# Optimization experiments

Hardware: AMD Instinct MI355X
Metric: run time of the kernel (lower is better)

Reference implementation:

```python
import jax, jax.numpy as jnp
import numpy as np

RANK = 3
NUM_STEPS = 3
NUM_ENT = 40000
NUM_EMB = 24
NUM_OPS = 12
DIM = 128
HID = 128
BATCH = 128
NNZ = 300000


def _lstm_dir(x, Wih, Whh, bih, bhh, reverse=False):
    # x: (S, B, D); PyTorch gate order i, f, g, o
    B = x.shape[1]
    H = Whh.shape[1]
    def step(carry, xt):
        h, c = carry
        z = xt @ Wih.T + h @ Whh.T + bih + bhh  # (B, 4H)
        i, f, g, o = jnp.split(z, 4, axis=-1)
        c = jax.nn.sigmoid(f) * c + jax.nn.sigmoid(i) * jnp.tanh(g)
        h = jax.nn.sigmoid(o) * jnp.tanh(c)
        return (h, c), h
    init = (jnp.zeros((B, H), x.dtype), jnp.zeros((B, H), x.dtype))
    _, hs = jax.lax.scan(step, init, x, reverse=reverse)
    return hs  # (S, B, H)


def _spmm(memory, src, dst, val, num_ent):
    # memory: (B, E); edges (src -> dst): out[b, j] = sum_{e: dst[e]=j} memory[b, src[e]] * val[e]
    g = memory[:, src] * val[None, :]              # (B, nnz)
    out = jax.ops.segment_sum(g.T, dst, num_segments=num_ent)  # (E, B)
    return out.T


def setup_inputs() -> dict:
    key = jax.random.key(0)
    ks = jax.random.split(key, 16)
    inp = {
        'queries': jax.random.randint(ks[0], (BATCH,), 0, NUM_EMB),
        'heads': jax.random.randint(ks[1], (BATCH,), 0, NUM_ENT),
        'edge_src': jax.random.randint(ks[2], (NUM_OPS, NNZ), 0, NUM_ENT, dtype=jnp.int32),
        'edge_dst': jax.random.randint(ks[3], (NUM_OPS, NNZ), 0, NUM_ENT, dtype=jnp.int32),
        'edge_val': jax.random.uniform(ks[4], (NUM_OPS, NNZ), jnp.float32),
        'emb': jax.random.normal(ks[5], (NUM_EMB, DIM), jnp.float32) * 0.1,
        'Wih_f': jax.random.normal(ks[6], (RANK, 4 * HID, DIM), jnp.float32) * 0.1,
        'Whh_f': jax.random.normal(ks[7], (RANK, 4 * HID, HID), jnp.float32) * 0.1,
        'bih_f': jnp.zeros((RANK, 4 * HID), jnp.float32),
        'bhh_f': jnp.zeros((RANK, 4 * HID), jnp.float32),
        'Wih_b': jax.random.normal(ks[8], (RANK, 4 * HID, DIM), jnp.float32) * 0.1,
        'Whh_b': jax.random.normal(ks[9], (RANK, 4 * HID, HID), jnp.float32) * 0.1,
        'bih_b': jnp.zeros((RANK, 4 * HID), jnp.float32),
        'bhh_b': jnp.zeros((RANK, 4 * HID), jnp.float32),
        'W0': jax.random.normal(ks[10], (2 * HID, NUM_OPS + 1), jnp.float32) * 0.1,
        'b0': jnp.zeros((1, NUM_OPS + 1), jnp.float32),
    }
    return inp


def reference(queries, heads, edge_src, edge_dst, edge_val, emb,
              Wih_f, Whh_f, bih_f, bhh_f, Wih_b, Whh_b, bih_b, bhh_b, W0, b0):
    # query embedding replicated over time: (S, B, D)
    q = emb[queries]
    x = jnp.broadcast_to(q[None], (NUM_STEPS, q.shape[0], q.shape[1]))
    head_onehot = jax.nn.one_hot(heads, NUM_ENT, dtype=jnp.float32)  # (B, E)

    logits = jnp.zeros((q.shape[0], NUM_ENT), jnp.float32)
    for r in range(RANK):
        hf = _lstm_dir(x, Wih_f[r], Whh_f[r], bih_f[r], bhh_f[r], reverse=False)
        hb = _lstm_dir(x, Wih_b[r], Whh_b[r], bih_b[r], bhh_b[r], reverse=True)
        rnn_out = jnp.concatenate([hf, hb], axis=-1)          # (S, B, 2H)
        trans = rnn_out @ W0 + b0                             # (S, B, ops+1)
        attn = jax.nn.softmax(trans, axis=-1)
        attn = jnp.transpose(attn, (0, 2, 1))                 # (S, ops+1, B)

        memory = head_onehot                                  # (B, E)
        for t in range(NUM_STEPS):
            attn_t = attn[t]                                  # (ops+1, B)
            acc = memory * attn_t[-1][:, None]                # identity operator
            for op in range(NUM_OPS):
                prod = _spmm(memory, edge_src[op], edge_dst[op], edge_val[op], NUM_ENT)
                acc = acc + prod * attn_t[op][:, None]
            memory = acc
        norm = jnp.maximum(jnp.float32(1e-20), jnp.sum(memory, axis=1, keepdims=True))
        logits = logits + memory / norm
    return logits
```

## Files before the change

### kernel.cpp

```cpp
#include <hip/hip_runtime.h>

#define NENT 40000
#define NB 128
#define NQ 24
#define NOPS 12
#define EPO 300000
#define NTOT (NOPS * EPO)
#define NRANK 3
#define NPASS 8
#define CP 16
#define ECAP 160

typedef float v4f __attribute__((ext_vector_type(4)));

__device__ __forceinline__ v4f shfl_xor4(v4f x, int m) {
    v4f r;
    r.x = __shfl_xor(x.x, m);
    r.y = __shfl_xor(x.y, m);
    r.z = __shfl_xor(x.z, m);
    r.w = __shfl_xor(x.w, m);
    return r;
}

__device__ __forceinline__ bool bittest(const unsigned* bm, int i) {
    return (bm[i >> 5] >> (i & 31)) & 1u;
}

__global__ void headmark_kernel(const int* __restrict__ heads, unsigned* __restrict__ bmH,
                                unsigned* __restrict__ bm2) {
    int h = heads[threadIdx.x];
    atomicOr(&bmH[h >> 5], 1u << (h & 31));
    atomicOr(&bm2[h >> 5], 1u << (h & 31));
}

__global__ void mark2_kernel(const int* __restrict__ src, const int* __restrict__ dst,
                             const unsigned* __restrict__ bmH, unsigned* __restrict__ bm2) {
    int i = blockIdx.x * 256 + threadIdx.x;
    if (i < NTOT) {
        int s = src[i];
        if (bittest(bmH, s)) {
            int d = dst[i];
            atomicOr(&bm2[d >> 5], 1u << (d & 31));
        }
    }
}

__global__ void build_ell_kernel(const int* __restrict__ src, const int* __restrict__ dst,
                                 const float* __restrict__ val, const unsigned* __restrict__ bm2,
                                 int* __restrict__ fillD, int* __restrict__ fillS,
                                 int2* __restrict__ eD, int2* __restrict__ eS) {
    int i = blockIdx.x * 256 + threadIdx.x;
    if (i >= NTOT) return;
    int s = src[i], d = dst[i];
    int op = i / EPO;
    int v = __float_as_int(val[i]);
    int pd = atomicAdd(&fillD[d], 1);
    eD[(size_t)d * ECAP + pd] = make_int2(s | (op << 16), v);
    if (bittest(bm2, s)) {
        int ps = atomicAdd(&fillS[s], 1);
        eS[(size_t)s * ECAP + ps] = make_int2(d | (op << 16), v);
    }
}

__global__ void zxq_kernel(const float* __restrict__ emb,
                           const float* __restrict__ Wih_f, const float* __restrict__ bih_f,
                           const float* __restrict__ bhh_f,
                           const float* __restrict__ Wih_b, const float* __restrict__ bih_b,
                           const float* __restrict__ bhh_b,
                           float* __restrict__ zxq) {
    int combo = blockIdx.x / NQ;
    int q = blockIdx.x % NQ;
    int dir = combo / 3, r = combo % 3;
    const float* Wih = (dir ? Wih_b : Wih_f) + r * 512 * 128;
    const float* bih = (dir ? bih_b : bih_f) + r * 512;
    const float* bhh = (dir ? bhh_b : bhh_f) + r * 512;
    __shared__ float x[128];
    int u = threadIdx.x;
    x[u] = emb[q * 128 + u];
    __syncthreads();
    const float* W0p = Wih + u * 128;
    const float* W1p = Wih + (128 + u) * 128;
    const float* W2p = Wih + (256 + u) * 128;
    const float* W3p = Wih + (384 + u) * 128;
    float a0 = 0.f, a1 = 0.f, a2 = 0.f, a3 = 0.f;
    for (int d = 0; d < 128; ++d) {
        float xv = x[d];
        a0 = fmaf(xv, W0p[d], a0);
        a1 = fmaf(xv, W1p[d], a1);
        a2 = fmaf(xv, W2p[d], a2);
        a3 = fmaf(xv, W3p[d], a3);
    }
    float* o = zxq + (size_t)(combo * NQ + q) * 512;
    o[u]       = a0 + bih[u]       + bhh[u];
    o[128 + u] = a1 + bih[128 + u] + bhh[128 + u];
    o[256 + u] = a2 + bih[256 + u] + bhh[256 + u];
    o[384 + u] = a3 + bih[384 + u] + bhh[384 + u];
}

__global__ void lstmq_kernel(const float* __restrict__ Whh_f, const float* __restrict__ Whh_b,
                             const float* __restrict__ zxq, float* __restrict__ hq) {
    int combo = blockIdx.x / NQ;
    int q = blockIdx.x % NQ;
    int dir = combo / 3, r = combo % 3;
    const float* Whh = (dir ? Whh_b : Whh_f) + r * 512 * 128;
    __shared__ float h[128];
    int u = threadIdx.x;
    const float* z = zxq + (size_t)(combo * NQ + q) * 512;
    float zi0 = z[u], zf0 = z[128 + u], zg0 = z[256 + u], zo0 = z[384 + u];
    const float* Wi = Whh + u * 128;
    const float* Wf = Whh + (128 + u) * 128;
    const float* Wg = Whh + (256 + u) * 128;
    const float* Wo = Whh + (384 + u) * 128;
    float c = 0.f;
    h[u] = 0.f;
    for (int s = 0; s < 3; ++s) {
        __syncthreads();
        float a0 = 0.f, a1 = 0.f, a2 = 0.f, a3 = 0.f;
        for (int d = 0; d < 128; ++d) {
            float hv = h[d];
            a0 = fmaf(hv, Wi[d], a0);
            a1 = fmaf(hv, Wf[d], a1);
            a2 = fmaf(hv, Wg[d], a2);
            a3 = fmaf(hv, Wo[d], a3);
        }
        float ig = 1.f / (1.f + expf(-(zi0 + a0)));
        float fg = 1.f / (1.f + expf(-(zf0 + a1)));
        float gg = tanhf(zg0 + a2);
        float og = 1.f / (1.f + expf(-(zo0 + a3)));
        c = fg * c + ig * gg;
        float hn = og * tanhf(c);
        __syncthreads();
        h[u] = hn;
        hq[(size_t)((combo * 3 + s) * NQ + q) * 128 + u] = hn;
    }
}

__global__ void attnq_kernel(const float* __restrict__ hq, const float* __restrict__ W0,
                             const float* __restrict__ b0, float* __restrict__ attnq) {
    int r = blockIdx.x / 3, t = blockIdx.x % 3;
    __shared__ float W0s[256 * 13];
    for (int idx = threadIdx.x; idx < 256 * 13; idx += 32) W0s[idx] = W0[idx];
    __syncthreads();
    int q = threadIdx.x;
    if (q >= NQ) return;
    float acc[13];
    for (int k = 0; k < 13; ++k) acc[k] = b0[k];
    const float* hf = hq + (size_t)(((0 * 3 + r) * 3 + t) * NQ + q) * 128;
    const float* hb = hq + (size_t)(((1 * 3 + r) * 3 + (2 - t)) * NQ + q) * 128;
    for (int u = 0; u < 128; ++u) {
        float v = hf[u];
        for (int k = 0; k < 13; ++k) acc[k] = fmaf(v, W0s[u * 13 + k], acc[k]);
    }
    for (int u = 0; u < 128; ++u) {
        float v = hb[u];
        for (int k = 0; k < 13; ++k) acc[k] = fmaf(v, W0s[(128 + u) * 13 + k], acc[k]);
    }
    float m = acc[0];
    for (int k = 1; k < 13; ++k) m = fmaxf(m, acc[k]);
    float e[13];
    float sum = 0.f;
    for (int k = 0; k < 13; ++k) { e[k] = expf(acc[k] - m); sum += e[k]; }
    float inv = 1.f / sum;
    float* ao = attnq + (size_t)(r * 3 + t) * 13 * NQ;
    for (int k = 0; k < 13; ++k) ao[k * NQ + q] = e[k] * inv;
}

__global__ void expand_kernel(const int* __restrict__ queries, const float* __restrict__ attnq,
                              float* __restrict__ attn) {
    __shared__ int qs[128];
    if (threadIdx.x < 128) qs[threadIdx.x] = queries[threadIdx.x];
    __syncthreads();
    for (int idx = threadIdx.x; idx < 9 * 13 * 128; idx += 256) {
        int b = idx & 127, kk = idx >> 7;
        attn[idx] = attnq[kk * NQ + qs[b]];
    }
}

__global__ void fused01_kernel(const int* __restrict__ heads, const float* __restrict__ attn,
                               const int* __restrict__ fillS, const int2* __restrict__ eS,
                               float* __restrict__ mem2) {
    int r = blockIdx.y;
    int b = blockIdx.x;
    int chunk = blockIdx.z;
    __shared__ float c0s[13], c1s[13];
    if (threadIdx.x < 13) {
        c0s[threadIdx.x] = attn[(size_t)((r * 3 + 0) * 13 + threadIdx.x) * 128 + b];
        c1s[threadIdx.x] = attn[(size_t)((r * 3 + 1) * 13 + threadIdx.x) * 128 + b];
    }
    __syncthreads();
    int h = heads[b];
    int lenH = fillS[h];
    float* mem = mem2 + ((size_t)(r * NPASS + (b >> 4)) * NENT) * CP + (b & 15);
    int g = threadIdx.x >> 3, lane8 = threadIdx.x & 7;
    for (int ent = g + chunk * 32; ent < lenH + 1; ent += 64) {
        int i; float wv;
        if (ent == 0) { i = h; wv = c0s[12]; }
        else {
            int2 e = eS[(size_t)h * ECAP + ent - 1];
            i = e.x & 0xFFFF;
            wv = __int_as_float(e.y) * c0s[e.x >> 16];
        }
        if (lane8 == 0) atomicAdd(&mem[(size_t)i * CP], c1s[12] * wv);
        int lenI = fillS[i];
        const int2* ei = eS + (size_t)i * ECAP;
        for (int f = lane8; f < lenI; f += 8) {
            int2 e2 = ei[f];
            atomicAdd(&mem[(size_t)(e2.x & 0xFFFF) * CP],
                      __int_as_float(e2.y) * c1s[e2.x >> 16] * wv);
        }
    }
}

struct Stage { v4f g0, g1, g2, g3; float w0, w1, w2, w3; int o0, o1, o2, o3; };

#define ISSUE_ONE(G, W, O, LT, RT, bi) { \
    bool m = (bi) < (LT); \
    int2 e = eL[RT][m ? (bi) : 0]; \
    int ex = m ? e.x : 0; \
    W = m ? __int_as_float(e.y) : 0.f; \
    O = ex >> 16; \
    G = *(const v4f*)(inr + (size_t)(ex & 0xFFFF) * CP + cq4); }

#define ISSUE(S, bb) { int bi = (bb) + slot; \
    ISSUE_ONE(S.g0, S.w0, S.o0, l0, rw + 0, bi) \
    ISSUE_ONE(S.g1, S.w1, S.o1, l1, rw + 1, bi) \
    ISSUE_ONE(S.g2, S.w2, S.o2, l2, rw + 2, bi) \
    ISSUE_ONE(S.g3, S.w3, S.o3, l3, rw + 3, bi) }

#define CONSUME(S) { \
    { v4f cc = *(const v4f*)&cs[S.o0 * 20 + cq4]; acc0 += (S.w0 * cc) * S.g0; } \
    { v4f cc = *(const v4f*)&cs[S.o1 * 20 + cq4]; acc1 += (S.w1 * cc) * S.g1; } \
    { v4f cc = *(const v4f*)&cs[S.o2 * 20 + cq4]; acc2 += (S.w2 * cc) * S.g2; } \
    { v4f cc = *(const v4f*)&cs[S.o3 * 20 + cq4]; acc3 += (S.w3 * cc) * S.g3; } }

#define REDUCE_ROW(A, T) { \
    v4f red = A; \
    red += shfl_xor4(red, 4); \
    red += shfl_xor4(red, 8); \
    red += shfl_xor4(red, 16); \
    red += shfl_xor4(red, 32); \
    if (slot == 0) { \
        int j = jw + (T); \
        v4f mi = *(const v4f*)(inr + (size_t)j * CP + cq4); \
        v4f res = cid * mi + red; \
        *(v4f*)(outr + (size_t)j * CP + cq4) = res; \
        rsum += res; \
    } }

__global__ __launch_bounds__(256) void dense_kernel(const float* __restrict__ attn,
                                                    const int* __restrict__ fillD,
                                                    const int2* __restrict__ edgesD,
                                                    const float* __restrict__ in,
                                                    float* __restrict__ out,
                                                    float* __restrict__ normv) {
    int p = blockIdx.x;
    int r = blockIdx.z;
    __shared__ __align__(16) float cs[13 * 20];
    __shared__ float npart[4][16];
    __shared__ __align__(16) int2 eL[16][ECAP];
    int tid = threadIdx.x;
    int wave = tid >> 6, lane = tid & 63;

    {
        const char* gp = (const char*)(edgesD + (size_t)(blockIdx.y * 16) * ECAP);
        char* lp = (char*)&eL[0][0];
#pragma unroll
        for (int k = 0; k < 5; ++k) {
            int off = (wave * 5 + k) * 1024;
            __builtin_amdgcn_global_load_lds(
                (const __attribute__((address_space(1))) unsigned*)(gp + off + lane * 16),
                (__attribute__((address_space(3))) unsigned*)(lp + off),
                16, 0, 0);
        }
    }
    if (tid < 13 * 16) {
        int op = tid >> 4, c0 = tid & 15;
        cs[op * 20 + c0] = attn[(size_t)((r * 3 + 2) * 13 + op) * 128 + p * CP + c0];
    }
    int slot = lane >> 2;
    int cq4 = (lane & 3) * 4;
    int rw = wave * 4;
    int jw = blockIdx.y * 16 + rw;
    int l0 = fillD[jw], l1 = fillD[jw + 1], l2 = fillD[jw + 2], l3 = fillD[jw + 3];
    int maxlen = max(max(l0, l1), max(l2, l3));
    const float* inr = in + (size_t)(r * NPASS + p) * NENT * CP;
    float* outr = out + (size_t)(r * NPASS + p) * NENT * CP;
    __syncthreads();

    v4f acc0 = (v4f)0.f, acc1 = (v4f)0.f, acc2 = (v4f)0.f, acc3 = (v4f)0.f;
    Stage SA, SB, SC;
    ISSUE(SA, 0)
    ISSUE(SB, 16)
    ISSUE(SC, 32)
    for (int base = 48; base < maxlen; base += 48) {
        CONSUME(SA) ISSUE(SA, base)
        CONSUME(SB) ISSUE(SB, base + 16)
        CONSUME(SC) ISSUE(SC, base + 32)
    }
    CONSUME(SA)
    CONSUME(SB)
    CONSUME(SC)

    v4f cid = *(const v4f*)&cs[12 * 20 + cq4];
    v4f rsum = (v4f)0.f;
    REDUCE_ROW(acc0, 0)
    REDUCE_ROW(acc1, 1)
    REDUCE_ROW(acc2, 2)
    REDUCE_ROW(acc3, 3)
    if (slot == 0) *(v4f*)&npart[wave][cq4] = rsum;
    __syncthreads();
    if (tid < 16) {
        float s = npart[0][tid] + npart[1][tid] + npart[2][tid] + npart[3][tid];
        atomicAdd(&normv[r * 128 + p * CP + tid], s);
    }
}

__global__ void rnorm_kernel(const float* __restrict__ normv, float* __restrict__ rnormv) {
    int i = threadIdx.x;
    rnormv[i] = 1.f / fmaxf(normv[i], 1e-20f);
}

__global__ void final_kernel(const float* __restrict__ mem3, const float* __restrict__ rnormv,
                             float* __restrict__ out) {
    __shared__ float tile[32 * 129];
    __shared__ float rn[384];
    for (int idx = threadIdx.x; idx < 384; idx += 256) rn[idx] = rnormv[idx];
    __syncthreads();
    int j0 = blockIdx.x * 32;
    for (int p = 0; p < NPASS; ++p) {
        for (int it = 0; it < 2; ++it) {
            int lin = it * 256 + threadIdx.x;
            int jj = lin >> 4, c = lin & 15;
            int b = p * CP + c;
            float s = 0.f;
            for (int r = 0; r < 3; ++r)
                s += mem3[((size_t)(r * NPASS + p) * NENT + j0 + jj) * CP + c] * rn[r * 128 + b];
            tile[jj * 129 + b] = s;
        }
    }
    __syncthreads();
    for (int it = 0; it < 16; ++it) {
        int lin = it * 256 + threadIdx.x;
        int b = lin >> 5, jj = lin & 31;
        out[(size_t)b * NENT + j0 + jj] = tile[jj * 129 + b];
    }
}

extern "C" void kernel_launch(void* const* d_in, const int* in_sizes, int n_in,
                              void* d_out, int out_size, void* d_ws, size_t ws_size,
                              hipStream_t stream) {
    const int*   queries  = (const int*)d_in[0];
    const int*   heads    = (const int*)d_in[1];
    const int*   edge_src = (const int*)d_in[2];
    const int*   edge_dst = (const int*)d_in[3];
    const float* edge_val = (const float*)d_in[4];
    const float* emb      = (const float*)d_in[5];
    const float* Wih_f    = (const float*)d_in[6];
    const float* Whh_f    = (const float*)d_in[7];
    const float* bih_f    = (const float*)d_in[8];
    const float* bhh_f    = (const float*)d_in[9];
    const float* Wih_b    = (const float*)d_in[10];
    const float* Whh_b    = (const float*)d_in[11];
    const float* bih_b    = (const float*)d_in[12];
    const float* bhh_b    = (const float*)d_in[13];
    const float* W0       = (const float*)d_in[14];
    const float* b0       = (const float*)d_in[15];
    float* out = (float*)d_out;

    char* w = (char*)d_ws;
    size_t off = 0;
    auto alloc = [&](size_t bytes) -> void* {
        off = (off + 255) & ~(size_t)255;
        void* p = w + off;
        off += bytes;
        return p;
    };
    float* attnq  = (float*)alloc((size_t)9 * 13 * NQ * sizeof(float));
    float* attn   = (float*)alloc((size_t)9 * 13 * 128 * sizeof(float));
    float* zxq    = (float*)alloc((size_t)6 * NQ * 512 * sizeof(float));
    float* hq     = (float*)alloc((size_t)6 * 3 * NQ * 128 * sizeof(float));
    unsigned* bmH = (unsigned*)alloc((2 * 1250 + 2 * NENT) * sizeof(int));
    unsigned* bm2 = bmH + 1250;
    int* fillD    = (int*)(bm2 + 1250);
    int* fillS    = fillD + NENT;
    int2*  eD     = (int2*)alloc((size_t)NENT * ECAP * sizeof(int2));
    float* mem2   = (float*)alloc((size_t)NRANK * NENT * NB * sizeof(float));
    float* mem3   = (float*)alloc((size_t)NRANK * NENT * NB * sizeof(float));
    int2*  eS     = (int2*)mem3;
    float* normv  = (float*)alloc((size_t)NRANK * NB * sizeof(float));
    float* rnormv = (float*)alloc((size_t)NRANK * NB * sizeof(float));

    int cooGrid = (NTOT + 255) / 256;

    hipMemsetAsync(bmH, 0, (2 * 1250 + 2 * NENT) * sizeof(int), stream);
    headmark_kernel<<<1, 128, 0, stream>>>(heads, bmH, bm2);
    mark2_kernel<<<cooGrid, 256, 0, stream>>>(edge_src, edge_dst, bmH, bm2);
    build_ell_kernel<<<cooGrid, 256, 0, stream>>>(edge_src, edge_dst, edge_val, bm2,
                                                  fillD, fillS, eD, eS);

    zxq_kernel<<<6 * NQ, 128, 0, stream>>>(emb, Wih_f, bih_f, bhh_f, Wih_b, bih_b, bhh_b, zxq);
    lstmq_kernel<<<6 * NQ, 128, 0, stream>>>(Whh_f, Whh_b, zxq, hq);
    attnq_kernel<<<9, 32, 0, stream>>>(hq, W0, b0, attnq);
    expand_kernel<<<1, 256, 0, stream>>>(queries, attnq, attn);

    hipMemsetAsync(mem2, 0, (size_t)NRANK * NENT * NB * sizeof(float), stream);
    hipMemsetAsync(normv, 0, NRANK * NB * sizeof(float), stream);
    {
        dim3 g(NB, NRANK, 2);
        fused01_kernel<<<g, 256, 0, stream>>>(heads, attn, fillS, eS, mem2);
    }
    {
        dim3 g(NPASS, NENT / 16, NRANK);
        dense_kernel<<<g, 256, 0, stream>>>(attn, fillD, eD, mem2, mem3, normv);
    }

    rnorm_kernel<<<1, NRANK * NB, 0, stream>>>(normv, rnormv);
    final_kernel<<<NENT / 32, 256, 0, stream>>>(mem3, rnormv, out);
}
```

Baseline: 1.444 ms.

## Stream edge lists from global memory with a two-level edge/gather software pipeline

Drops the up-front global_load_lds staging of each block's 16 edge lists into LDS. Edges are now loaded straight from global memory into registers, one stage ahead of the dependent row gathers, in a rotating three-buffer pipeline. This removes the LDS footprint and the startup wait on the bulk copy, and should raise occupancy. In exchange, the gather addresses now depend on global edge loads inside the loop, which lengthens the dependency chain and adds register pressure.

```diff
diff --git a/kernel.cpp b/kernel.cpp
--- a/kernel.cpp
+++ b/kernel.cpp
@@ -211,27 +211,30 @@
     }
 }
 
-struct Stage { v4f g0, g1, g2, g3; float w0, w1, w2, w3; int o0, o1, o2, o3; };
-
-#define ISSUE_ONE(G, W, O, LT, RT, bi) { \
-    bool m = (bi) < (LT); \
-    int2 e = eL[RT][m ? (bi) : 0]; \
-    int ex = m ? e.x : 0; \
-    W = m ? __int_as_float(e.y) : 0.f; \
-    O = ex >> 16; \
-    G = *(const v4f*)(inr + (size_t)(ex & 0xFFFF) * CP + cq4); }
-
-#define ISSUE(S, bb) { int bi = (bb) + slot; \
-    ISSUE_ONE(S.g0, S.w0, S.o0, l0, rw + 0, bi) \
-    ISSUE_ONE(S.g1, S.w1, S.o1, l1, rw + 1, bi) \
-    ISSUE_ONE(S.g2, S.w2, S.o2, l2, rw + 2, bi) \
-    ISSUE_ONE(S.g3, S.w3, S.o3, l3, rw + 3, bi) }
-
-#define CONSUME(S) { \
-    { v4f cc = *(const v4f*)&cs[S.o0 * 20 + cq4]; acc0 += (S.w0 * cc) * S.g0; } \
-    { v4f cc = *(const v4f*)&cs[S.o1 * 20 + cq4]; acc1 += (S.w1 * cc) * S.g1; } \
-    { v4f cc = *(const v4f*)&cs[S.o2 * 20 + cq4]; acc2 += (S.w2 * cc) * S.g2; } \
-    { v4f cc = *(const v4f*)&cs[S.o3 * 20 + cq4]; acc3 += (S.w3 * cc) * S.g3; } }
+struct EStage { int2 a, b, c, d; };
+struct GStage { v4f a, b, c, d; };
+
+#define ISSUE_E(E, bb) { int bi = (bb) + slot; \
+    E.a = edp0[bi < l0 ? bi : 0]; \
+    E.b = edp1[bi < l1 ? bi : 0]; \
+    E.c = edp2[bi < l2 ? bi : 0]; \
+    E.d = edp3[bi < l3 ? bi : 0]; }
+
+#define ISSUE_G(G, E) { \
+    G.a = *(const v4f*)(inr + (size_t)(E.a.x & 0xFFFF) * CP + cq4); \
+    G.b = *(const v4f*)(inr + (size_t)(E.b.x & 0xFFFF) * CP + cq4); \
+    G.c = *(const v4f*)(inr + (size_t)(E.c.x & 0xFFFF) * CP + cq4); \
+    G.d = *(const v4f*)(inr + (size_t)(E.d.x & 0xFFFF) * CP + cq4); }
+
+#define CONSUME_P(G, E, bb) { int bi = (bb) + slot; \
+    { v4f cc = *(const v4f*)&cs[(E.a.x >> 16) * 20 + cq4]; \
+      float w = bi < l0 ? __int_as_float(E.a.y) : 0.f; acc0 += (w * cc) * G.a; } \
+    { v4f cc = *(const v4f*)&cs[(E.b.x >> 16) * 20 + cq4]; \
+      float w = bi < l1 ? __int_as_float(E.b.y) : 0.f; acc1 += (w * cc) * G.b; } \
+    { v4f cc = *(const v4f*)&cs[(E.c.x >> 16) * 20 + cq4]; \
+      float w = bi < l2 ? __int_as_float(E.c.y) : 0.f; acc2 += (w * cc) * G.c; } \
+    { v4f cc = *(const v4f*)&cs[(E.d.x >> 16) * 20 + cq4]; \
+      float w = bi < l3 ? __int_as_float(E.d.y) : 0.f; acc3 += (w * cc) * G.d; } }
 
 #define REDUCE_ROW(A, T) { \
     v4f red = A; \
@@ -257,49 +260,47 @@
     int r = blockIdx.z;
     __shared__ __align__(16) float cs[13 * 20];
     __shared__ float npart[4][16];
-    __shared__ __align__(16) int2 eL[16][ECAP];
     int tid = threadIdx.x;
-    int wave = tid >> 6, lane = tid & 63;
-
-    {
-        const char* gp = (const char*)(edgesD + (size_t)(blockIdx.y * 16) * ECAP);
-        char* lp = (char*)&eL[0][0];
-#pragma unroll
-        for (int k = 0; k < 5; ++k) {
-            int off = (wave * 5 + k) * 1024;
-            __builtin_amdgcn_global_load_lds(
-                (const __attribute__((address_space(1))) unsigned*)(gp + off + lane * 16),
-                (__attribute__((address_space(3))) unsigned*)(lp + off),
-                16, 0, 0);
-        }
-    }
     if (tid < 13 * 16) {
         int op = tid >> 4, c0 = tid & 15;
         cs[op * 20 + c0] = attn[(size_t)((r * 3 + 2) * 13 + op) * 128 + p * CP + c0];
     }
+    __syncthreads();
+    int wave = tid >> 6, lane = tid & 63;
     int slot = lane >> 2;
     int cq4 = (lane & 3) * 4;
-    int rw = wave * 4;
-    int jw = blockIdx.y * 16 + rw;
-    int l0 = fillD[jw], l1 = fillD[jw + 1], l2 = fillD[jw + 2], l3 = fillD[jw + 3];
-    int maxlen = max(max(l0, l1), max(l2, l3));
+    int jw = blockIdx.y * 16 + wave * 4;
     const float* inr = in + (size_t)(r * NPASS + p) * NENT * CP;
     float* outr = out + (size_t)(r * NPASS + p) * NENT * CP;
-    __syncthreads();
-
+    int l0 = fillD[jw], l1 = fillD[jw + 1], l2 = fillD[jw + 2], l3 = fillD[jw + 3];
+    const int2* edp0 = edgesD + (size_t)(jw + 0) * ECAP;
+    const int2* edp1 = edgesD + (size_t)(jw + 1) * ECAP;
+    const int2* edp2 = edgesD + (size_t)(jw + 2) * ECAP;
+    const int2* edp3 = edgesD + (size_t)(jw + 3) * ECAP;
+    int maxlen = max(max(l0, l1), max(l2, l3));
     v4f acc0 = (v4f)0.f, acc1 = (v4f)0.f, acc2 = (v4f)0.f, acc3 = (v4f)0.f;
-    Stage SA, SB, SC;
-    ISSUE(SA, 0)
-    ISSUE(SB, 16)
-    ISSUE(SC, 32)
-    for (int base = 48; base < maxlen; base += 48) {
-        CONSUME(SA) ISSUE(SA, base)
-        CONSUME(SB) ISSUE(SB, base + 16)
-        CONSUME(SC) ISSUE(SC, base + 32)
-    }
-    CONSUME(SA)
-    CONSUME(SB)
-    CONSUME(SC)
+
+    EStage E0, E1, E2;
+    GStage G0, G1, G2;
+    ISSUE_E(E0, 0)
+    ISSUE_E(E1, 16)
+    ISSUE_E(E2, 32)
+    ISSUE_G(G0, E0)
+    ISSUE_G(G1, E1)
+    int nb = (maxlen + 15) >> 4;
+    int R = (nb + 2) / 3;
+    int base = 0;
+    for (int rr = 0; rr < R; ++rr, base += 48) {
+        CONSUME_P(G0, E0, base)
+        ISSUE_E(E0, base + 48)
+        ISSUE_G(G2, E2)
+        CONSUME_P(G1, E1, base + 16)
+        ISSUE_E(E1, base + 64)
+        ISSUE_G(G0, E0)
+        CONSUME_P(G2, E2, base + 32)
+        ISSUE_E(E2, base + 80)
+        ISSUE_G(G1, E1)
+    }
 
     v4f cid = *(const v4f*)&cs[12 * 20 + cq4];
     v4f rsum = (v4f)0.f;
```

After: 1.271 ms. 1.14x faster.
